# Optimization experiments

Hardware: AMD Instinct MI355X
Metric: run time of the kernel (lower is better)

## Reference

```python
import jax, jax.numpy as jnp
import numpy as np

GRID_SIZE, K, NUM_EXPERTS = 5, 3, 8
N_MLP, N_KAN = 4, 4
B, D, H, O = 4096, 512, 2048, 512


def _bspline_basis(x, grid, k):
    """Cox-de Boor recursion, vectorized. x: [B, D]; grid: [G]. Returns [B, D, G-k-1]."""
    xe = x[..., None]
    # order-0: indicator of grid interval
    b = ((grid[:-1] <= xe) & (xe < grid[1:])).astype(x.dtype)  # [B, D, G-1]
    for kk in range(1, k + 1):
        t_i = grid[: -(kk + 1)]
        t_ik = grid[kk:-1]
        t_ik1 = grid[kk + 1:]
        t_i1 = grid[1:-kk]
        left = (xe - t_i) / (t_ik - t_i) * b[..., :-1]
        right = (t_ik1 - xe) / (t_ik1 - t_i1) * b[..., 1:]
        b = left + right
    return b


def setup_inputs() -> dict:
    key = jax.random.key(0)
    ks = jax.random.split(key, 8)
    x = jax.random.normal(ks[0], (B, D), dtype=jnp.float32)
    # Router output: binary expert mask; rows with no active group fall back to expert 7
    mask = (jax.random.uniform(ks[1], (B, NUM_EXPERTS)) < 0.3).astype(jnp.float32)
    other = jnp.zeros((NUM_EXPERTS,), jnp.float32).at[7].set(1.0)
    expert_mask = jnp.where(mask.sum(axis=1, keepdims=True) == 0, other[None, :], mask)
    s_d = 1.0 / np.sqrt(D)
    s_h = 1.0 / np.sqrt(H)
    gate_w = jax.random.normal(ks[2], (D, NUM_EXPERTS), jnp.float32) * s_d
    gate_b = jnp.zeros((NUM_EXPERTS,), jnp.float32)
    mlp_w1 = jax.random.normal(ks[3], (N_MLP, D, H), jnp.float32) * s_d
    mlp_b1 = jnp.zeros((N_MLP, H), jnp.float32)
    mlp_w2 = jax.random.normal(ks[4], (N_MLP, H, O), jnp.float32) * s_h
    mlp_b2 = jnp.zeros((N_MLP, O), jnp.float32)
    kan_scaling = jnp.ones((N_KAN, D, O), jnp.float32)
    kan_coeff = jax.random.normal(ks[5], (N_KAN, D, O, GRID_SIZE + K), jnp.float32)
    return dict(x=x, expert_mask=expert_mask, gate_w=gate_w, gate_b=gate_b,
                mlp_w1=mlp_w1, mlp_b1=mlp_b1, mlp_w2=mlp_w2, mlp_b2=mlp_b2,
                kan_scaling=kan_scaling, kan_coeff=kan_coeff)


def reference(x, expert_mask, gate_w, gate_b, mlp_w1, mlp_b1, mlp_w2, mlp_b2,
              kan_scaling, kan_coeff):
    # gate softmax + router mask + renormalize
    gate = jax.nn.softmax(x @ gate_w + gate_b, axis=1)          # [B, E]
    masked = gate * expert_mask
    w = masked / (masked.sum(axis=1, keepdims=True) + 1e-9)      # [B, E]

    # MLP experts (eval mode -> dropout is identity)
    h = jax.nn.relu(jnp.einsum('bd,edh->ebh', x, mlp_w1) + mlp_b1[:, None, :])
    mlp_out = jnp.einsum('ebh,eho->ebo', h, mlp_w2) + mlp_b2[:, None, :]  # [4, B, O]

    # KAN experts: uniform grid extended by k knots each side (spacing 2/grid_size)
    hg = 2.0 / GRID_SIZE
    grid = jnp.arange(GRID_SIZE + 2 * K + 1, dtype=x.dtype) * hg - (1.0 + K * hg)
    basis = _bspline_basis(x, grid, K)                           # [B, D, 8]
    ceff = kan_coeff * kan_scaling[..., None]                    # [4, D, O, 8]
    kan_out = jnp.einsum('big,eiog->ebo', basis, ceff)           # [4, B, O]

    expert_outputs = jnp.concatenate([mlp_out, kan_out], axis=0)  # [8, B, O]
    out = jnp.einsum('ebo,be->bo', expert_outputs, w)             # [B, O]
    return out, expert_mask, w
```

## Files before the change

kernel.cpp:

```cpp
#include <hip/hip_runtime.h>

typedef __attribute__((ext_vector_type(4))) float f32x4;
typedef __attribute__((ext_vector_type(8))) __bf16 bf16x8;
typedef __attribute__((ext_vector_type(4))) unsigned short u16x4;
typedef __attribute__((ext_vector_type(8))) unsigned short u16x8;

#define NB 4096
#define ND 512
#define NH 2048
#define NO 512

__device__ __forceinline__ unsigned short f2bf(float f) {
  unsigned int u = __float_as_uint(f);
  u += 0x7fffu + ((u >> 16) & 1u);
  return (unsigned short)(u >> 16);
}
__device__ __forceinline__ float bf2f(unsigned short u) {
  return __uint_as_float(((unsigned int)u) << 16);
}
__device__ __forceinline__ void gload_lds16(const void* g, void* l) {
  __builtin_amdgcn_global_load_lds(
      (const __attribute__((address_space(1))) unsigned int*)g,
      (__attribute__((address_space(3))) unsigned int*)l, 16, 0, 0);
}

__global__ void gate_kernel(const float* __restrict__ x, const float* __restrict__ emask,
                            const float* __restrict__ gw, const float* __restrict__ gb,
                            float* __restrict__ w_out, float* __restrict__ mask_out) {
  int b = blockIdx.x;
  int lane = threadIdx.x;
  float l8[8] = {0,0,0,0,0,0,0,0};
  const float* xr = x + (size_t)b * ND;
  for (int d = lane; d < ND; d += 64) {
    float xv = xr[d];
    const float* g = gw + d * 8;
#pragma unroll
    for (int e = 0; e < 8; ++e) l8[e] = fmaf(xv, g[e], l8[e]);
  }
#pragma unroll
  for (int off = 32; off > 0; off >>= 1) {
#pragma unroll
    for (int e = 0; e < 8; ++e) l8[e] += __shfl_xor(l8[e], off);
  }
  float m = -1e30f;
#pragma unroll
  for (int e = 0; e < 8; ++e) { l8[e] += gb[e]; m = fmaxf(m, l8[e]); }
  float s = 0.f, p[8];
#pragma unroll
  for (int e = 0; e < 8; ++e) { p[e] = expf(l8[e] - m); s += p[e]; }
  float inv = 1.f / s;
  float mk[8], me[8], ms = 0.f;
#pragma unroll
  for (int e = 0; e < 8; ++e) {
    mk[e] = emask[(size_t)b * 8 + e];
    me[e] = p[e] * inv * mk[e];
    ms += me[e];
  }
  float winv = 1.f / (ms + 1e-9f);
  if (lane == 0) {
#pragma unroll
    for (int e = 0; e < 8; ++e) {
      w_out[(size_t)b * 8 + e] = me[e] * winv;
      mask_out[(size_t)b * 8 + e] = mk[e];
    }
  }
}

__global__ void cast_x_kernel(const float* __restrict__ x, unsigned short* __restrict__ xb) {
  size_t i = ((size_t)blockIdx.x * 256 + threadIdx.x) * 4;
  f32x4 v = *(const f32x4*)(x + i);
  u16x4 r;
#pragma unroll
  for (int j = 0; j < 4; ++j) r[j] = f2bf(v[j]);
  *(u16x4*)(xb + i) = r;
}

__global__ void basis_kernel(const float* __restrict__ x, unsigned short* __restrict__ bas) {
  size_t t = (size_t)blockIdx.x * 256 + threadIdx.x;
  float xv = x[t];
  const float hg = 0.4f;
  float tt[12];
#pragma unroll
  for (int j = 0; j < 12; ++j) tt[j] = -2.2f + hg * (float)j;
  float b0[11];
#pragma unroll
  for (int j = 0; j < 11; ++j) b0[j] = (tt[j] <= xv && xv < tt[j + 1]) ? 1.f : 0.f;
  float b1[10], b2[9], b3[8];
#pragma unroll
  for (int j = 0; j < 10; ++j) b1[j] = ((xv - tt[j]) * b0[j] + (tt[j + 2] - xv) * b0[j + 1]) * (1.f / (1.f * hg));
#pragma unroll
  for (int j = 0; j < 9; ++j)  b2[j] = ((xv - tt[j]) * b1[j] + (tt[j + 3] - xv) * b1[j + 1]) * (1.f / (2.f * hg));
#pragma unroll
  for (int j = 0; j < 8; ++j)  b3[j] = ((xv - tt[j]) * b2[j] + (tt[j + 4] - xv) * b2[j + 1]) * (1.f / (3.f * hg));
  u16x8 r;
#pragma unroll
  for (int j = 0; j < 8; ++j) r[j] = f2bf(b3[j]);
  *(u16x8*)(bas + t * 8) = r;
}

__global__ void transpose_cast(const float* __restrict__ in, unsigned short* __restrict__ outp,
                               int R, int Cc) {
  __shared__ float tile[32][33];
  int e = blockIdx.z;
  int c0 = blockIdx.x * 32, r0 = blockIdx.y * 32;
  int tx = threadIdx.x & 31, ty = threadIdx.x >> 5;
  const float* ine = in + (size_t)e * R * Cc;
  unsigned short* oute = outp + (size_t)e * R * Cc;
#pragma unroll
  for (int j = 0; j < 32; j += 8)
    tile[ty + j][tx] = ine[(size_t)(r0 + ty + j) * Cc + (c0 + tx)];
  __syncthreads();
#pragma unroll
  for (int j = 0; j < 32; j += 8)
    oute[(size_t)(c0 + ty + j) * R + (r0 + tx)] = f2bf(tile[tx][ty + j]);
}

__global__ void make_cefft(const float* __restrict__ coeff, const float* __restrict__ scal,
                           unsigned short* __restrict__ outp) {
  size_t t = (size_t)blockIdx.x * 256 + threadIdx.x;
  int i = (int)(t & 511);
  int o = (int)((t >> 9) & 511);
  int e = (int)(t >> 18);
  size_t io = ((size_t)e * 512 + i) * 512 + o;
  const f32x4* cp = (const f32x4*)(coeff + io * 8);
  f32x4 c0 = cp[0], c1 = cp[1];
  float s = scal[io];
  u16x8 r;
#pragma unroll
  for (int j = 0; j < 4; ++j) r[j] = f2bf(c0[j] * s);
#pragma unroll
  for (int j = 0; j < 4; ++j) r[4 + j] = f2bf(c1[j] * s);
  *(u16x8*)(outp + ((size_t)e * 512 + o) * 4096 + (size_t)i * 8) = r;
}

template <int MODE>
__global__ __launch_bounds__(512, 2) void gemm_bt(
    const unsigned short* __restrict__ A, size_t strideAe, int lda,
    const unsigned short* __restrict__ Bm, size_t strideBe, int ldb,
    const float* __restrict__ bias, int strideBiasE,
    unsigned short* __restrict__ C, size_t strideCe, int ldc, int K) {
  __shared__ __align__(16) char lsA[3 * 32768];
  __shared__ __align__(16) char lsB[3 * 16384];
  const int tid = threadIdx.x;
  const int lane = tid & 63, wid = tid >> 6;
  const int wr = wid >> 1, wc = wid & 1;
  const int gx = gridDim.x;
  const int nxy = gx * gridDim.y;
  int flat = blockIdx.y * gx + blockIdx.x;
  flat = (flat & 7) * (nxy >> 3) + (flat >> 3);
  const int brow = (flat / gx) * 256, bcol = (flat % gx) * 128;
  const int e = blockIdx.z;
  const unsigned short* Ae = A + (size_t)e * strideAe;
  const unsigned short* Be = Bm + (size_t)e * strideBe;
  const int NT = K >> 6;

  const int fr = lane & 15, fc = lane >> 4;
  const int swz = fr & 7;
  const int sR = tid >> 3, ssc = tid & 7;

  auto issueA = [&](int buf, int t2, int q) {
    int R = q * 64 + sR;
    gload_lds16(Ae + (size_t)(brow + R) * lda + (size_t)(t2 * 64 + ((ssc ^ (R & 7)) << 3)),
                lsA + buf * 32768 + q * 8192 + tid * 16);
  };
  auto issueB = [&](int buf, int t2, int q) {
    int R = q * 64 + sR;
    gload_lds16(Be + (size_t)(bcol + R) * ldb + (size_t)(t2 * 64 + ((ssc ^ (R & 7)) << 3)),
                lsB + buf * 16384 + q * 8192 + tid * 16);
  };

  f32x4 acc[4][4] = {};

  issueA(0, 0, 0); issueA(0, 0, 1); issueA(0, 0, 2); issueA(0, 0, 3);
  issueB(0, 0, 0); issueB(0, 0, 1);
  issueA(1, 1, 0); issueA(1, 1, 1); issueA(1, 1, 2); issueA(1, 1, 3);
  issueB(1, 1, 0); issueB(1, 1, 1);
  asm volatile("s_waitcnt vmcnt(6)" ::: "memory");
  __builtin_amdgcn_s_barrier();

  int bi = 0;
  for (int t = 0; t < NT; ++t) {
    char* bA = lsA + bi * 32768;
    char* bB = lsB + bi * 16384;
    int pb = (bi == 0) ? 2 : bi - 1;
    const bool pf = (t + 2 < NT);

    bf16x8 af[4], bfrag[4];
#pragma unroll
    for (int i = 0; i < 4; ++i) {
      int ra = wr * 64 + i * 16 + fr;
      af[i] = *(const bf16x8*)(bA + ra * 128 + ((fc ^ swz) << 4));
      int rb = wc * 64 + i * 16 + fr;
      bfrag[i] = *(const bf16x8*)(bB + rb * 128 + ((fc ^ swz) << 4));
    }
    if (pf) { issueA(pb, t + 2, 0); issueA(pb, t + 2, 1); issueA(pb, t + 2, 2); }
    __builtin_amdgcn_s_barrier();
    asm volatile("s_waitcnt lgkmcnt(0)" ::: "memory");
    __builtin_amdgcn_sched_barrier(0);
    __builtin_amdgcn_s_setprio(1);
#pragma unroll
    for (int mi = 0; mi < 4; ++mi)
#pragma unroll
      for (int ni = 0; ni < 4; ++ni)
        acc[mi][ni] = __builtin_amdgcn_mfma_f32_16x16x32_bf16(bfrag[ni], af[mi], acc[mi][ni], 0, 0, 0);
    __builtin_amdgcn_s_setprio(0);
    __builtin_amdgcn_s_barrier();

#pragma unroll
    for (int i = 0; i < 4; ++i) {
      int ra = wr * 64 + i * 16 + fr;
      af[i] = *(const bf16x8*)(bA + ra * 128 + (((4 + fc) ^ swz) << 4));
      int rb = wc * 64 + i * 16 + fr;
      bfrag[i] = *(const bf16x8*)(bB + rb * 128 + (((4 + fc) ^ swz) << 4));
    }
    if (pf) { issueA(pb, t + 2, 3); issueB(pb, t + 2, 0); issueB(pb, t + 2, 1); }
    __builtin_amdgcn_s_barrier();
    asm volatile("s_waitcnt lgkmcnt(0)" ::: "memory");
    __builtin_amdgcn_sched_barrier(0);
    __builtin_amdgcn_s_setprio(1);
#pragma unroll
    for (int mi = 0; mi < 4; ++mi)
#pragma unroll
      for (int ni = 0; ni < 4; ++ni)
        acc[mi][ni] = __builtin_amdgcn_mfma_f32_16x16x32_bf16(bfrag[ni], af[mi], acc[mi][ni], 0, 0, 0);
    __builtin_amdgcn_s_setprio(0);
    if (pf) asm volatile("s_waitcnt vmcnt(6)" ::: "memory");
    else    asm volatile("s_waitcnt vmcnt(0)" ::: "memory");
    __builtin_amdgcn_s_barrier();

    bi = (bi == 2) ? 0 : bi + 1;
  }

  unsigned short* Ce = C + (size_t)e * strideCe;
#pragma unroll
  for (int mi = 0; mi < 4; ++mi) {
    int row = brow + wr * 64 + mi * 16 + fr;
#pragma unroll
    for (int ni = 0; ni < 4; ++ni) {
      int col0 = bcol + wc * 64 + ni * 16 + (fc << 2);
      f32x4 bv = {0.f, 0.f, 0.f, 0.f};
      if constexpr (MODE != 2) bv = *(const f32x4*)(bias + e * strideBiasE + col0);
      u16x4 r;
#pragma unroll
      for (int j = 0; j < 4; ++j) {
        float v = acc[mi][ni][j] + bv[j];
        if constexpr (MODE == 0) v = fmaxf(v, 0.f);
        r[j] = f2bf(v);
      }
      *(u16x4*)(Ce + (size_t)row * ldc + col0) = r;
    }
  }
}

__global__ void combine_kernel(const unsigned short* __restrict__ eo,
                               const float* __restrict__ w, float* __restrict__ out) {
  int b = blockIdx.x;
  int o = threadIdx.x * 4;
  float wv[8];
#pragma unroll
  for (int e = 0; e < 8; ++e) wv[e] = w[(size_t)b * 8 + e];
  f32x4 acc = {0.f, 0.f, 0.f, 0.f};
#pragma unroll
  for (int e = 0; e < 8; ++e) {
    u16x4 u = *(const u16x4*)(eo + ((size_t)e * NB + b) * NO + o);
#pragma unroll
    for (int j = 0; j < 4; ++j) acc[j] = fmaf(wv[e], bf2f(u[j]), acc[j]);
  }
  *(f32x4*)(out + (size_t)b * NO + o) = acc;
}

extern "C" void kernel_launch(void* const* d_in, const int* in_sizes, int n_in,
                              void* d_out, int out_size, void* d_ws, size_t ws_size,
                              hipStream_t stream) {
  (void)in_sizes; (void)n_in; (void)out_size; (void)ws_size;
  const float* x      = (const float*)d_in[0];
  const float* emask  = (const float*)d_in[1];
  const float* gate_w = (const float*)d_in[2];
  const float* gate_b = (const float*)d_in[3];
  const float* mlp_w1 = (const float*)d_in[4];
  const float* mlp_b1 = (const float*)d_in[5];
  const float* mlp_w2 = (const float*)d_in[6];
  const float* mlp_b2 = (const float*)d_in[7];
  const float* kan_s  = (const float*)d_in[8];
  const float* kan_c  = (const float*)d_in[9];

  float* out = (float*)d_out;
  float* mask_out = out + (size_t)NB * NO;
  float* w_out    = mask_out + (size_t)NB * 8;

  char* ws = (char*)d_ws;
  size_t off = 0;
  auto take = [&](size_t bytes) { size_t r = off; off += (bytes + 255) & ~(size_t)255; return r; };
  unsigned short* w1t   = (unsigned short*)(ws + take((size_t)4 * NH * ND * 2));
  unsigned short* w2t   = (unsigned short*)(ws + take((size_t)4 * NO * NH * 2));
  unsigned short* cefft = (unsigned short*)(ws + take((size_t)4 * NO * (ND * 8) * 2));
  unsigned short* xbf   = (unsigned short*)(ws + take((size_t)NB * ND * 2));
  unsigned short* eo    = (unsigned short*)(ws + take((size_t)8 * NB * NO * 2));
  unsigned short* hbuf  = (unsigned short*)(ws + take((size_t)4 * NB * NH * 2));
  unsigned short* bas   = hbuf;

  gate_kernel<<<NB, 64, 0, stream>>>(x, emask, gate_w, gate_b, w_out, mask_out);
  cast_x_kernel<<<(NB * ND) / (256 * 4), 256, 0, stream>>>(x, xbf);
  transpose_cast<<<dim3(NH / 32, ND / 32, 4), 256, 0, stream>>>(mlp_w1, w1t, ND, NH);
  transpose_cast<<<dim3(NO / 32, NH / 32, 4), 256, 0, stream>>>(mlp_w2, w2t, NH, NO);
  make_cefft<<<(4 * ND * NO) / 256, 256, 0, stream>>>(kan_c, kan_s, cefft);

  gemm_bt<0><<<dim3(NH / 128, NB / 256, 4), 512, 0, stream>>>(
      xbf, 0, ND,
      w1t, (size_t)NH * ND, ND,
      mlp_b1, NH,
      hbuf, (size_t)NB * NH, NH, ND);
  gemm_bt<1><<<dim3(NO / 128, NB / 256, 4), 512, 0, stream>>>(
      hbuf, (size_t)NB * NH, NH,
      w2t, (size_t)NO * NH, NH,
      mlp_b2, NO,
      eo, (size_t)NB * NO, NO, NH);
  basis_kernel<<<(NB * ND) / 256, 256, 0, stream>>>(x, bas);
  gemm_bt<2><<<dim3(NO / 128, NB / 256, 4), 512, 0, stream>>>(
      bas, 0, ND * 8,
      cefft, (size_t)NO * (ND * 8), ND * 8,
      nullptr, 0,
      eo + (size_t)4 * NB * NO, (size_t)NB * NO, NO, ND * 8);

  combine_kernel<<<NB, NO / 4, 0, stream>>>(eo, w_out, out);
}
```

Baseline: 235.5 us.

## Shrink GEMM tiles to 128x128 with K-step 32 and 256-thread blocks

Reworks the bf16 GEMM from 256x128 tiles with 8 waves and a 64-wide K step into 128x128 tiles with 4 waves and a 32-wide K step. It uses a new LDS swizzle and a simplified single-phase triple-buffered pipeline. The aim is more blocks and higher occupancy (3 per CU) with less LDS per block, which should improve load balance across CUs. The trade-off is lower arithmetic intensity per tile and more barriers per unit of K work.

```diff
diff --git a/kernel.cpp b/kernel.cpp
--- a/kernel.cpp
+++ b/kernel.cpp
@@ -134,13 +134,13 @@
 }
 
 template <int MODE>
-__global__ __launch_bounds__(512, 2) void gemm_bt(
+__global__ __launch_bounds__(256, 3) void gemm_bt(
     const unsigned short* __restrict__ A, size_t strideAe, int lda,
     const unsigned short* __restrict__ Bm, size_t strideBe, int ldb,
     const float* __restrict__ bias, int strideBiasE,
     unsigned short* __restrict__ C, size_t strideCe, int ldc, int K) {
-  __shared__ __align__(16) char lsA[3 * 32768];
-  __shared__ __align__(16) char lsB[3 * 16384];
+  __shared__ __align__(16) char lsA[3 * 8192];
+  __shared__ __align__(16) char lsB[3 * 8192];
   const int tid = threadIdx.x;
   const int lane = tid & 63, wid = tid >> 6;
   const int wr = wid >> 1, wc = wid & 1;
@@ -148,52 +148,55 @@
   const int nxy = gx * gridDim.y;
   int flat = blockIdx.y * gx + blockIdx.x;
   flat = (flat & 7) * (nxy >> 3) + (flat >> 3);
-  const int brow = (flat / gx) * 256, bcol = (flat % gx) * 128;
+  const int brow = (flat / gx) * 128, bcol = (flat % gx) * 128;
   const int e = blockIdx.z;
   const unsigned short* Ae = A + (size_t)e * strideAe;
   const unsigned short* Be = Bm + (size_t)e * strideBe;
-  const int NT = K >> 6;
+  const int NT = K >> 5;
 
   const int fr = lane & 15, fc = lane >> 4;
-  const int swz = fr & 7;
-  const int sR = tid >> 3, ssc = tid & 7;
-
-  auto issueA = [&](int buf, int t2, int q) {
-    int R = q * 64 + sR;
-    gload_lds16(Ae + (size_t)(brow + R) * lda + (size_t)(t2 * 64 + ((ssc ^ (R & 7)) << 3)),
-                lsA + buf * 32768 + q * 8192 + tid * 16);
+  const int sR = tid >> 2, ssc = tid & 3;
+
+  auto stage = [&](int buf, int t2) {
+#pragma unroll
+    for (int q = 0; q < 2; ++q) {
+      int R = q * 64 + sR;
+      int kk = t2 * 32 + ((ssc ^ ((R >> 1) & 3)) << 3);
+      gload_lds16(Ae + (size_t)(brow + R) * lda + (size_t)kk,
+                  lsA + buf * 8192 + q * 4096 + tid * 16);
+    }
+#pragma unroll
+    for (int q = 0; q < 2; ++q) {
+      int R = q * 64 + sR;
+      int kk = t2 * 32 + ((ssc ^ ((R >> 1) & 3)) << 3);
+      gload_lds16(Be + (size_t)(bcol + R) * ldb + (size_t)kk,
+                  lsB + buf * 8192 + q * 4096 + tid * 16);
+    }
   };
-  auto issueB = [&](int buf, int t2, int q) {
-    int R = q * 64 + sR;
-    gload_lds16(Be + (size_t)(bcol + R) * ldb + (size_t)(t2 * 64 + ((ssc ^ (R & 7)) << 3)),
-                lsB + buf * 16384 + q * 8192 + tid * 16);
-  };
 
   f32x4 acc[4][4] = {};
 
-  issueA(0, 0, 0); issueA(0, 0, 1); issueA(0, 0, 2); issueA(0, 0, 3);
-  issueB(0, 0, 0); issueB(0, 0, 1);
-  issueA(1, 1, 0); issueA(1, 1, 1); issueA(1, 1, 2); issueA(1, 1, 3);
-  issueB(1, 1, 0); issueB(1, 1, 1);
-  asm volatile("s_waitcnt vmcnt(6)" ::: "memory");
+  stage(0, 0);
+  stage(1, 1);
+  asm volatile("s_waitcnt vmcnt(4)" ::: "memory");
   __builtin_amdgcn_s_barrier();
 
   int bi = 0;
   for (int t = 0; t < NT; ++t) {
-    char* bA = lsA + bi * 32768;
-    char* bB = lsB + bi * 16384;
-    int pb = (bi == 0) ? 2 : bi - 1;
+    const char* bA = lsA + bi * 8192;
+    const char* bB = lsB + bi * 8192;
+    const int pb = (bi == 0) ? 2 : bi - 1;
     const bool pf = (t + 2 < NT);
 
     bf16x8 af[4], bfrag[4];
 #pragma unroll
     for (int i = 0; i < 4; ++i) {
       int ra = wr * 64 + i * 16 + fr;
-      af[i] = *(const bf16x8*)(bA + ra * 128 + ((fc ^ swz) << 4));
+      af[i] = *(const bf16x8*)(bA + ra * 64 + ((fc ^ ((ra >> 1) & 3)) << 4));
       int rb = wc * 64 + i * 16 + fr;
-      bfrag[i] = *(const bf16x8*)(bB + rb * 128 + ((fc ^ swz) << 4));
-    }
-    if (pf) { issueA(pb, t + 2, 0); issueA(pb, t + 2, 1); issueA(pb, t + 2, 2); }
+      bfrag[i] = *(const bf16x8*)(bB + rb * 64 + ((fc ^ ((rb >> 1) & 3)) << 4));
+    }
+    if (pf) stage(pb, t + 2);
     __builtin_amdgcn_s_barrier();
     asm volatile("s_waitcnt lgkmcnt(0)" ::: "memory");
     __builtin_amdgcn_sched_barrier(0);
@@ -204,28 +207,8 @@
       for (int ni = 0; ni < 4; ++ni)
         acc[mi][ni] = __builtin_amdgcn_mfma_f32_16x16x32_bf16(bfrag[ni], af[mi], acc[mi][ni], 0, 0, 0);
     __builtin_amdgcn_s_setprio(0);
-    __builtin_amdgcn_s_barrier();
-
-#pragma unroll
-    for (int i = 0; i < 4; ++i) {
-      int ra = wr * 64 + i * 16 + fr;
-      af[i] = *(const bf16x8*)(bA + ra * 128 + (((4 + fc) ^ swz) << 4));
-      int rb = wc * 64 + i * 16 + fr;
-      bfrag[i] = *(const bf16x8*)(bB + rb * 128 + (((4 + fc) ^ swz) << 4));
-    }
-    if (pf) { issueA(pb, t + 2, 3); issueB(pb, t + 2, 0); issueB(pb, t + 2, 1); }
-    __builtin_amdgcn_s_barrier();
-    asm volatile("s_waitcnt lgkmcnt(0)" ::: "memory");
-    __builtin_amdgcn_sched_barrier(0);
-    __builtin_amdgcn_s_setprio(1);
-#pragma unroll
-    for (int mi = 0; mi < 4; ++mi)
-#pragma unroll
-      for (int ni = 0; ni < 4; ++ni)
-        acc[mi][ni] = __builtin_amdgcn_mfma_f32_16x16x32_bf16(bfrag[ni], af[mi], acc[mi][ni], 0, 0, 0);
-    __builtin_amdgcn_s_setprio(0);
-    if (pf) asm volatile("s_waitcnt vmcnt(6)" ::: "memory");
-    else    asm volatile("s_waitcnt vmcnt(0)" ::: "memory");
+    if (pf)               asm volatile("s_waitcnt vmcnt(4)" ::: "memory");
+    else if (t + 1 < NT)  asm volatile("s_waitcnt vmcnt(0)" ::: "memory");
     __builtin_amdgcn_s_barrier();
 
     bi = (bi == 2) ? 0 : bi + 1;
@@ -305,18 +288,18 @@
   transpose_cast<<<dim3(NO / 32, NH / 32, 4), 256, 0, stream>>>(mlp_w2, w2t, NH, NO);
   make_cefft<<<(4 * ND * NO) / 256, 256, 0, stream>>>(kan_c, kan_s, cefft);
 
-  gemm_bt<0><<<dim3(NH / 128, NB / 256, 4), 512, 0, stream>>>(
+  gemm_bt<0><<<dim3(NH / 128, NB / 128, 4), 256, 0, stream>>>(
       xbf, 0, ND,
       w1t, (size_t)NH * ND, ND,
       mlp_b1, NH,
       hbuf, (size_t)NB * NH, NH, ND);
-  gemm_bt<1><<<dim3(NO / 128, NB / 256, 4), 512, 0, stream>>>(
+  gemm_bt<1><<<dim3(NO / 128, NB / 128, 4), 256, 0, stream>>>(
       hbuf, (size_t)NB * NH, NH,
       w2t, (size_t)NO * NH, NH,
       mlp_b2, NO,
       eo, (size_t)NB * NO, NO, NH);
   basis_kernel<<<(NB * ND) / 256, 256, 0, stream>>>(x, bas);
-  gemm_bt<2><<<dim3(NO / 128, NB / 256, 4), 512, 0, stream>>>(
+  gemm_bt<2><<<dim3(NO / 128, NB / 128, 4), 256, 0, stream>>>(
       bas, 0, ND * 8,
       cefft, (size_t)NO * (ND * 8), ND * 8,
       nullptr, 0,
```

Measured after the change: 242.9 us. 3.1% more time.
